# Performance work log

Hardware: AMD Instinct MI355X
Metric: run time of the kernel (lower is better)

Reference implementation:

```python
import jax, jax.numpy as jnp
import numpy as np

NG, NL, NCAM, NP, ED = 8, 4, 6, 7, 256  # groups, levels, cams, key points, embed dims
GD = ED // NG
FIX_SCALE = jnp.array([[0.0, 0.0, 0.0], [0.45, 0.0, 0.0], [-0.45, 0.0, 0.0],
                       [0.0, 0.45, 0.0], [0.0, -0.45, 0.0], [0.0, 0.0, 0.45],
                       [0.0, 0.0, -0.45]], dtype=jnp.float32)


def grid_sample_bilinear(feat, grid):
    """feat [N,C,H,W], grid [N,A,P,2] in [-1,1]; bilinear, zeros padding, align_corners=False."""
    N, C, H, W = feat.shape
    A, P = grid.shape[1], grid.shape[2]
    gx = (grid[..., 0] + 1.0) * (W * 0.5) - 0.5
    gy = (grid[..., 1] + 1.0) * (H * 0.5) - 0.5
    x0 = jnp.floor(gx)
    y0 = jnp.floor(gy)
    wx1 = gx - x0
    wy1 = gy - y0
    feat_flat = feat.reshape(N, C, H * W)

    def gather(xi, yi, w):
        valid = (xi >= 0) & (xi <= W - 1) & (yi >= 0) & (yi <= H - 1)
        xc = jnp.clip(xi, 0, W - 1).astype(jnp.int32)
        yc = jnp.clip(yi, 0, H - 1).astype(jnp.int32)
        idx = (yc * W + xc).reshape(N, 1, A * P)
        vals = jnp.take_along_axis(feat_flat, idx, axis=2)  # [N,C,A*P]
        return vals * (w * valid).reshape(N, 1, A * P)

    out = (gather(x0, y0, (1.0 - wx1) * (1.0 - wy1))
           + gather(x0 + 1.0, y0, wx1 * (1.0 - wy1))
           + gather(x0, y0 + 1.0, (1.0 - wx1) * wy1)
           + gather(x0 + 1.0, y0 + 1.0, wx1 * wy1))
    return out.reshape(N, C, A, P)


def _forward(instance_feature, anchor, anchor_embed, feat0, feat1, feat2, feat3,
             projection_mat, image_wh, w_fc, b_fc, w_out, b_out):
    B, A = anchor.shape[:2]
    # --- key point generation (box_code_size=8: size + yaw rotation + translation) ---
    size = jnp.exp(anchor[..., 3:6])[:, :, None, :]           # [B,A,1,3]
    kp = FIX_SCALE * size                                      # [B,A,7,3]
    sin, cos = anchor[..., 6], anchor[..., 7]
    z = jnp.zeros_like(cos)
    o = jnp.ones_like(cos)
    rot = jnp.stack([jnp.stack([cos, -sin, z], -1),
                     jnp.stack([sin, cos, z], -1),
                     jnp.stack([z, z, o], -1)], -2)            # [B,A,3,3]
    kp = jnp.einsum('baij,bapj->bapi', rot, kp) + anchor[..., None, 0:3]

    # --- attention weights: softmax over cams*levels*pts per group ---
    feature = instance_feature + anchor_embed
    w = feature @ w_fc.T + b_fc                                # [B,A,NG*NCAM*NL*NP]
    w = jax.nn.softmax(w.reshape(B, A, NCAM * NL * NP, NG), axis=2)
    w = w.reshape(B, A, NCAM, NL, NP, NG)

    # --- project key points to normalized image coords ---
    pts = jnp.concatenate([kp, jnp.ones_like(kp[..., :1])], -1)  # [B,A,7,4]
    p2d = jnp.einsum('bcij,bapj->bcapi', projection_mat, pts)[..., :3]
    xy = p2d[..., :2] / jnp.maximum(p2d[..., 2:3], 1e-5)
    xy = xy / jnp.maximum(image_wh[:, :, None, None], 1e-5)
    grid = (xy * 2.0 - 1.0).reshape(B * NCAM, A, NP, 2)

    # --- multilevel bilinear sampling ---
    levels = [feat0, feat1, feat2, feat3]
    sampled = jnp.stack([grid_sample_bilinear(f.reshape((B * NCAM,) + f.shape[2:]), grid)
                         for f in levels], axis=1)             # [B*Ncam,NL,C,A,P]
    feats = sampled.reshape(B, NCAM, NL, ED, A, NP).transpose(0, 4, 1, 2, 5, 3)  # [B,A,Ncam,NL,P,C]
    feats = feats.reshape(B, A, NCAM, NL, NP, NG, GD)

    # --- weighted fusion over cams, levels, then sum over key points ---
    fused = jnp.einsum('bacnpgd,bacnpg->bagd', feats, w).reshape(B, A, ED)
    return fused @ w_out.T + b_out


def setup_inputs() -> dict:
    ks = jax.random.split(jax.random.key(0), 13)
    B, A = 2, 900
    return {
        'instance_feature': jax.random.normal(ks[0], (B, A, ED), jnp.float32),
        'anchor': jax.random.normal(ks[1], (B, A, 8), jnp.float32),
        'anchor_embed': jax.random.normal(ks[2], (B, A, ED), jnp.float32),
        'feat0': jax.random.normal(ks[3], (B, NCAM, ED, 64, 176), jnp.float32),
        'feat1': jax.random.normal(ks[4], (B, NCAM, ED, 32, 88), jnp.float32),
        'feat2': jax.random.normal(ks[5], (B, NCAM, ED, 16, 44), jnp.float32),
        'feat3': jax.random.normal(ks[6], (B, NCAM, ED, 8, 22), jnp.float32),
        'projection_mat': jax.random.normal(ks[7], (B, NCAM, 4, 4), jnp.float32),
        'image_wh': jnp.ones((B, NCAM, 2), jnp.float32),
        'w_fc': jax.random.normal(ks[8], (NG * NCAM * NL * NP, ED), jnp.float32) * 0.02,
        'b_fc': jax.random.normal(ks[9], (NG * NCAM * NL * NP,), jnp.float32) * 0.02,
        'w_out': jax.random.normal(ks[10], (ED, ED), jnp.float32) * 0.02,
        'b_out': jax.random.normal(ks[11], (ED,), jnp.float32) * 0.02,
    }


def reference(instance_feature, anchor, anchor_embed, feat0, feat1, feat2, feat3,
              projection_mat, image_wh, w_fc, b_fc, w_out, b_out):
    return _forward(instance_feature, anchor, anchor_embed, feat0, feat1, feat2, feat3,
                    projection_mat, image_wh, w_fc, b_fc, w_out, b_out)
```

## Files before the change

kernel.cpp:

```cpp
#include <hip/hip_runtime.h>
#include <math.h>

constexpr int B = 2, A = 900, ED = 256, NG = 8, NCAM = 6, NL = 4, NP = 7;
constexpr int NJ = NG * NCAM * NL * NP;
constexpr int NBA = B * A;
constexpr int NE = NCAM * NL * NP;
constexpr int LDST = 260;

__constant__ float FIXS[NP][3] = {
  {0.f,0.f,0.f},{0.45f,0.f,0.f},{-0.45f,0.f,0.f},
  {0.f,0.45f,0.f},{0.f,-0.45f,0.f},{0.f,0.f,0.45f},{0.f,0.f,-0.45f}};

__constant__ int cH[NL]  = {64,32,16,8};
__constant__ int cW[NL]  = {176,88,44,22};
__constant__ int cHW[NL] = {11264,2816,704,176};
__constant__ long long cLOFF[NL] = {0LL, 0LL, 8650752LL, 10813440LL};

__global__ __launch_bounds__(256) void k_tr_cl(
    const float* __restrict__ f1, const float* __restrict__ f2,
    const float* __restrict__ f3, float* __restrict__ tfeat)
{
  __shared__ float tile[32 * LDST];
  const int bc = blockIdx.y;
  const int bx = blockIdx.x;
  int lvl, t0;
  if      (bx < 88)  { lvl = 1; t0 = 0; }
  else if (bx < 110) { lvl = 2; t0 = 88; }
  else               { lvl = 3; t0 = 110; }
  const int HW  = cHW[lvl];
  const int px0 = (bx - t0) * 32;
  const float* in = ((lvl==1)?f1:(lvl==2)?f2:f3) + (size_t)bc * ED * HW + px0;
  float* outp = tfeat + cLOFF[lvl] + ((size_t)bc * HW + px0) * ED;
  const int t = threadIdx.x;
  const int npx = min(32, HW - px0);

#pragma unroll
  for (int j = 0; j < 8; ++j) {
    const int px = 4 * j;
    if (px < npx) {
      const float4 v = *(const float4*)(in + (size_t)t * HW + px);
      tile[(px+0)*LDST + t] = v.x;
      tile[(px+1)*LDST + t] = v.y;
      tile[(px+2)*LDST + t] = v.z;
      tile[(px+3)*LDST + t] = v.w;
    }
  }
  __syncthreads();
  const int wv = t >> 6, l = t & 63;
  for (int px = wv; px < npx; px += 4) {
    const float4 v = *(const float4*)&tile[px*LDST + 4*l];
    *(float4*)(outp + (size_t)px * ED + 4*l) = v;
  }
}

__global__ __launch_bounds__(256) void k_tr(const float* __restrict__ in,
                                            float* __restrict__ out, int R, int C)
{
  __shared__ float tile[32][33];
  const int r0 = blockIdx.y * 32, c0 = blockIdx.x * 32;
  const int tx = threadIdx.x, ty = threadIdx.y;
#pragma unroll
  for (int kk = 0; kk < 4; ++kk) {
    const int r = r0 + ty + kk*8, c = c0 + tx;
    if (r < R && c < C) tile[ty + kk*8][tx] = in[(size_t)r*C + c];
  }
  __syncthreads();
#pragma unroll
  for (int kk = 0; kk < 4; ++kk) {
    const int c = c0 + ty + kk*8, r = r0 + tx;
    if (r < R && c < C) out[(size_t)c*R + r] = tile[tx][ty + kk*8];
  }
}

__global__ __launch_bounds__(192) void k_fc(const float* __restrict__ inst,
    const float* __restrict__ emb, const float* __restrict__ wt,
    const float* __restrict__ b_fc, float* __restrict__ wraw)
{
  __shared__ float fsh[8][ED];
  const int a0 = blockIdx.x * 8;
  const int j  = blockIdx.y * 192 + threadIdx.x;
  const int t  = threadIdx.x;

  for (int i = t; i < 8 * ED; i += 192) {
    const int a = i >> 8, k = i & 255;
    const size_t idx = (size_t)(a0 + a) * ED + k;
    fsh[a][k] = inst[idx] + emb[idx];
  }
  __syncthreads();

  float acc[8] = {0.f,0.f,0.f,0.f,0.f,0.f,0.f,0.f};
  for (int k = 0; k < ED; k += 4) {
    float w0 = wt[(size_t)(k+0)*NJ + j];
    float w1 = wt[(size_t)(k+1)*NJ + j];
    float w2 = wt[(size_t)(k+2)*NJ + j];
    float w3 = wt[(size_t)(k+3)*NJ + j];
#pragma unroll
    for (int a = 0; a < 8; ++a)
      acc[a] += w0*fsh[a][k] + w1*fsh[a][k+1] + w2*fsh[a][k+2] + w3*fsh[a][k+3];
  }
  const float bj = b_fc[j];
#pragma unroll
  for (int a = 0; a < 8; ++a)
    wraw[(size_t)(a0+a)*NJ + j] = acc[a] + bj;
}

template<bool CL>
__global__ __launch_bounds__(256) void k_sample_h(
    const float* __restrict__ anchor, const float* __restrict__ proj,
    const float* __restrict__ wh, const float* __restrict__ wraw,
    const float* __restrict__ tfeat,
    const float* __restrict__ f0, const float* __restrict__ f1,
    const float* __restrict__ f2, const float* __restrict__ f3,
    float* __restrict__ fused)
{
  __shared__ float wsh[NJ];
  __shared__ float gridsh[NCAM][NP][2];
  __shared__ const float* cbase[NE];
  __shared__ float4 cwt[NE];
  __shared__ int4   cmeta[NE];
  __shared__ int wcnt[4];

  const int ba = blockIdx.x;
  const int b  = ba / A;
  const int t  = threadIdx.x;

  for (int j = t; j < NJ; j += 256)
    wsh[(j & 7) * NE + (j >> 3)] = wraw[(size_t)ba*NJ + j];

  if (t < NCAM*NP) {
    const int c = t / NP, p = t % NP;
    const float* an = anchor + (size_t)ba * 8;
    const float sx = expf(an[3]), sy = expf(an[4]), sz = expf(an[5]);
    const float sn = an[6], cs = an[7];
    const float kx = FIXS[p][0]*sx, ky = FIXS[p][1]*sy, kz = FIXS[p][2]*sz;
    const float px = cs*kx - sn*ky + an[0];
    const float py = sn*kx + cs*ky + an[1];
    const float pz = kz + an[2];
    const float* P = proj + ((size_t)(b*NCAM + c))*16;
    const float X = P[0]*px + P[1]*py + P[2]*pz  + P[3];
    const float Y = P[4]*px + P[5]*py + P[6]*pz  + P[7];
    const float Z = P[8]*px + P[9]*py + P[10]*pz + P[11];
    const float zc  = fmaxf(Z, 1e-5f);
    const float whx = fmaxf(wh[(b*NCAM+c)*2+0], 1e-5f);
    const float why = fmaxf(wh[(b*NCAM+c)*2+1], 1e-5f);
    gridsh[c][p][0] = (X/zc/whx)*2.f - 1.f;
    gridsh[c][p][1] = (Y/zc/why)*2.f - 1.f;
  }
  __syncthreads();

  bool valid = false;
  int fl = 0, dx = 0, dy = 0, chstep = 0;
  float wx1 = 0.f, wy1 = 0.f;
  const float* bptr = nullptr;
  if (t < NE) {
    const int c = t / (NL*NP); const int r = t % (NL*NP);
    const int l = r / NP, p = r % NP;
    const int Wl = cW[l], Hl = cH[l], HWl = cHW[l];
    const float gx = (gridsh[c][p][0] + 1.f) * (Wl * 0.5f) - 0.5f;
    const float gy = (gridsh[c][p][1] + 1.f) * (Hl * 0.5f) - 0.5f;
    const float x0f = floorf(gx), y0f = floorf(gy);
    const bool vx0 = (x0f >=  0.f) & (x0f <= (float)(Wl-1));
    const bool vx1 = (x0f >= -1.f) & (x0f <= (float)(Wl-2));
    const bool vy0 = (y0f >=  0.f) & (y0f <= (float)(Hl-1));
    const bool vy1 = (y0f >= -1.f) & (y0f <= (float)(Hl-2));
    fl = ((vx0&&vy0)?1:0) | ((vx1&&vy0)?2:0) | ((vx0&&vy1)?4:0) | ((vx1&&vy1)?8:0);
    if (fl) {
      wx1 = gx - x0f; wy1 = gy - y0f;
      const int x0 = (int)x0f, y0 = (int)y0f;
      if (CL && l >= 1) {
        bptr = tfeat + cLOFF[l]
             + ((size_t)(b*NCAM + c) * HWl + (long long)(y0*Wl + x0)) * ED;
        chstep = 1; dx = ED; dy = Wl * ED;
      } else {
        const float* fp = (l==0)?f0:(l==1)?f1:(l==2)?f2:f3;
        bptr = fp + (size_t)(b*NCAM + c) * ED * HWl + (long long)(y0*Wl + x0);
        chstep = HWl; dx = 1; dy = Wl;
      }
      valid = true;
    }
  }

  const unsigned long long mask = __ballot(valid);
  const int lane = t & 63, wv = t >> 6;
  if (lane == 0) wcnt[wv] = __popcll(mask);
  __syncthreads();
  int off = 0, nv = 0;
#pragma unroll
  for (int i = 0; i < 4; ++i) { if (i < wv) off += wcnt[i]; nv += wcnt[i]; }
  if (valid) {
    const int pos = off + __popcll(mask & ((1ull << lane) - 1ull));
    cbase[pos] = bptr;
    cwt[pos]   = make_float4((1.f-wx1)*(1.f-wy1), wx1*(1.f-wy1),
                             (1.f-wx1)*wy1,       wx1*wy1);
    cmeta[pos] = make_int4(dx, dy, fl | (t << 8), chstep);
  }

  {
    const int g = t >> 5, ln = t & 31;
    float* wg = wsh + g * NE;
    float m = -3.4e38f;
    for (int i = ln; i < NE; i += 32) m = fmaxf(m, wg[i]);
#pragma unroll
    for (int mk = 16; mk >= 1; mk >>= 1) m = fmaxf(m, __shfl_xor(m, mk));
    float s = 0.f;
    for (int i = ln; i < NE; i += 32) {
      const float e = expf(wg[i] - m);
      wg[i] = e;
      s += e;
    }
#pragma unroll
    for (int mk = 16; mk >= 1; mk >>= 1) s += __shfl_xor(s, mk);
    const float inv = 1.f / s;
    for (int i = ln; i < NE; i += 32) wg[i] *= inv;
  }
  __syncthreads();

  float acc = 0.f;
  const int g = t >> 5;
  for (int i = 0; i < nv; ++i) {
    const int4 m = cmeta[i];
    const float* pb = cbase[i] + (size_t)t * m.w;
    const float4 w4 = cwt[i];
    const float aw = wsh[g*NE + (m.z >> 8)];
    const int f = m.z & 255;
    float sv = 0.f;
    if (f == 15) {
      sv = w4.x*pb[0] + w4.y*pb[m.x] + w4.z*pb[m.y] + w4.w*pb[m.x+m.y];
    } else {
      if (f & 1) sv += w4.x*pb[0];
      if (f & 2) sv += w4.y*pb[m.x];
      if (f & 4) sv += w4.z*pb[m.y];
      if (f & 8) sv += w4.w*pb[m.x+m.y];
    }
    acc += aw * sv;
  }
  fused[(size_t)ba*ED + t] = acc;
}

__global__ __launch_bounds__(256) void k_out(const float* __restrict__ fused,
    const float* __restrict__ w_out, const float* __restrict__ b_out,
    float* __restrict__ out)
{
  __shared__ float fsh[8][ED];
  const int a0 = blockIdx.x * 8;
  const int t = threadIdx.x;
#pragma unroll
  for (int k = 0; k < 8; ++k) fsh[k][t] = fused[(size_t)(a0+k)*ED + t];
  __syncthreads();
  float acc[8] = {0.f,0.f,0.f,0.f,0.f,0.f,0.f,0.f};
  for (int i = 0; i < ED; i += 4) {
    const float4 w4 = *(const float4*)&w_out[(size_t)t*ED + i];
#pragma unroll
    for (int k = 0; k < 8; ++k) {
      const float4 fv = *(const float4*)&fsh[k][i];
      acc[k] += w4.x*fv.x + w4.y*fv.y + w4.z*fv.z + w4.w*fv.w;
    }
  }
  const float bo = b_out[t];
#pragma unroll
  for (int k = 0; k < 8; ++k) out[(size_t)(a0+k)*ED + t] = acc[k] + bo;
}

extern "C" void kernel_launch(void* const* d_in, const int* in_sizes, int n_in,
                              void* d_out, int out_size, void* d_ws, size_t ws_size,
                              hipStream_t stream) {
  const float* inst   = (const float*)d_in[0];
  const float* anchor = (const float*)d_in[1];
  const float* emb    = (const float*)d_in[2];
  const float* f0 = (const float*)d_in[3];
  const float* f1 = (const float*)d_in[4];
  const float* f2 = (const float*)d_in[5];
  const float* f3 = (const float*)d_in[6];
  const float* proj  = (const float*)d_in[7];
  const float* wh    = (const float*)d_in[8];
  const float* w_fc  = (const float*)d_in[9];
  const float* b_fc  = (const float*)d_in[10];
  const float* w_out = (const float*)d_in[11];
  const float* b_out = (const float*)d_in[12];
  float* out = (float*)d_out;
  float* ws  = (float*)d_ws;

  const size_t TFEAT = 11354112ULL;
  const size_t WRAW  = (size_t)NBA * NJ;
  const size_t FUSED = (size_t)NBA * ED;
  const size_t WT    = (size_t)ED * NJ;
  const bool tr = ws_size >= (TFEAT + WRAW + FUSED + WT) * sizeof(float);

  float* tfeat  = ws;
  float* wraw   = tr ? (ws + TFEAT) : ws;
  float* fusedp = wraw + WRAW;
  float* wt     = fusedp + FUSED;

  k_tr<<<dim3(ED/32, NJ/32, 1), dim3(32,8), 0, stream>>>(w_fc, wt, NJ, ED);

  if (tr)
    k_tr_cl<<<dim3(116, B*NCAM), 256, 0, stream>>>(f1, f2, f3, tfeat);

  k_fc<<<dim3(NBA / 8, 7), 192, 0, stream>>>(inst, emb, wt, b_fc, wraw);

  if (tr)
    k_sample_h<true><<<NBA, 256, 0, stream>>>(anchor, proj, wh, wraw, tfeat,
                                              f0, f1, f2, f3, fusedp);
  else
    k_sample_h<false><<<NBA, 256, 0, stream>>>(anchor, proj, wh, wraw, tfeat,
                                               f0, f1, f2, f3, fusedp);

  k_out<<<NBA / 8, 256, 0, stream>>>(fusedp, w_out, b_out, out);
}
```

Measured before the change: 380.8 us.

## Split sampling kernel across two blocks per anchor and use branchless clamped corner gathers

The sampling kernel now launches two blocks per anchor, each handling half of the camera/level/point samples. Partial sums go to two separate fused buffers, which the output projection kernel adds together. The per-sample flag branches are replaced with four precomputed clamped corner pointers and zeroed weights, so the inner loop is branchless and unrolled. This gives more blocks and memory parallelism, at the cost of recomputing the softmax and grid setup in both halves, plus extra workspace and fused traffic.

```diff
diff --git a/kernel.cpp b/kernel.cpp
--- a/kernel.cpp
+++ b/kernel.cpp
@@ -6,6 +6,8 @@
 constexpr int NBA = B * A;
 constexpr int NE = NCAM * NL * NP;
 constexpr int LDST = 260;
+constexpr int SPLIT = 2;
+constexpr int EHALF = NE / SPLIT;
 
 __constant__ float FIXS[NP][3] = {
   {0.f,0.f,0.f},{0.45f,0.f,0.f},{-0.45f,0.f,0.f},
@@ -115,14 +117,15 @@
 {
   __shared__ float wsh[NJ];
   __shared__ float gridsh[NCAM][NP][2];
-  __shared__ const float* cbase[NE];
-  __shared__ float4 cwt[NE];
-  __shared__ int4   cmeta[NE];
+  __shared__ const float* cptr[EHALF][4];
+  __shared__ float4 cwt[EHALF];
+  __shared__ int2   cmeta[EHALF];
   __shared__ int wcnt[4];
 
-  const int ba = blockIdx.x;
-  const int b  = ba / A;
-  const int t  = threadIdx.x;
+  const int ba   = blockIdx.x;
+  const int half = blockIdx.y;
+  const int b    = ba / A;
+  const int t    = threadIdx.x;
 
   for (int j = t; j < NJ; j += 256)
     wsh[(j & 7) * NE + (j >> 3)] = wraw[(size_t)ba*NJ + j];
@@ -149,11 +152,12 @@
   __syncthreads();
 
   bool valid = false;
-  int fl = 0, dx = 0, dy = 0, chstep = 0;
-  float wx1 = 0.f, wy1 = 0.f;
-  const float* bptr = nullptr;
-  if (t < NE) {
-    const int c = t / (NL*NP); const int r = t % (NL*NP);
+  int chstep = 0;
+  float4 w4 = make_float4(0.f,0.f,0.f,0.f);
+  const float *p00=nullptr, *p10=nullptr, *p01=nullptr, *p11=nullptr;
+  const int e = half * EHALF + t;
+  if (t < EHALF) {
+    const int c = e / (NL*NP); const int r = e % (NL*NP);
     const int l = r / NP, p = r % NP;
     const int Wl = cW[l], Hl = cH[l], HWl = cHW[l];
     const float gx = (gridsh[c][p][0] + 1.f) * (Wl * 0.5f) - 0.5f;
@@ -163,20 +167,33 @@
     const bool vx1 = (x0f >= -1.f) & (x0f <= (float)(Wl-2));
     const bool vy0 = (y0f >=  0.f) & (y0f <= (float)(Hl-1));
     const bool vy1 = (y0f >= -1.f) & (y0f <= (float)(Hl-2));
-    fl = ((vx0&&vy0)?1:0) | ((vx1&&vy0)?2:0) | ((vx0&&vy1)?4:0) | ((vx1&&vy1)?8:0);
-    if (fl) {
-      wx1 = gx - x0f; wy1 = gy - y0f;
-      const int x0 = (int)x0f, y0 = (int)y0f;
-      if (CL && l >= 1) {
-        bptr = tfeat + cLOFF[l]
-             + ((size_t)(b*NCAM + c) * HWl + (long long)(y0*Wl + x0)) * ED;
-        chstep = 1; dx = ED; dy = Wl * ED;
-      } else {
-        const float* fp = (l==0)?f0:(l==1)?f1:(l==2)?f2:f3;
-        bptr = fp + (size_t)(b*NCAM + c) * ED * HWl + (long long)(y0*Wl + x0);
-        chstep = HWl; dx = 1; dy = Wl;
+    if (vx0|vx1|vy0|vy1) {
+      const float wx1 = gx - x0f, wy1 = gy - y0f;
+      const int x0 = (int)fmaxf(fminf(x0f,        (float)(Wl-1)), 0.f);
+      const int x1 = (int)fmaxf(fminf(x0f + 1.f,  (float)(Wl-1)), 0.f);
+      const int y0 = (int)fmaxf(fminf(y0f,        (float)(Hl-1)), 0.f);
+      const int y1 = (int)fmaxf(fminf(y0f + 1.f,  (float)(Hl-1)), 0.f);
+      w4 = make_float4((1.f-wx1)*(1.f-wy1)*(vx0&&vy0),
+                       wx1*(1.f-wy1)*(vx1&&vy0),
+                       (1.f-wx1)*wy1*(vx0&&vy1),
+                       wx1*wy1*(vx1&&vy1));
+      if (w4.x != 0.f || w4.y != 0.f || w4.z != 0.f || w4.w != 0.f) {
+        const float* base;
+        int estep;
+        if (CL && l >= 1) {
+          base = tfeat + cLOFF[l] + (size_t)(b*NCAM + c) * HWl * ED;
+          estep = ED; chstep = 1;
+        } else {
+          const float* fp = (l==0)?f0:(l==1)?f1:(l==2)?f2:f3;
+          base = fp + (size_t)(b*NCAM + c) * ED * HWl;
+          estep = 1; chstep = HWl;
+        }
+        p00 = base + (size_t)(y0*Wl + x0) * estep;
+        p10 = base + (size_t)(y0*Wl + x1) * estep;
+        p01 = base + (size_t)(y1*Wl + x0) * estep;
+        p11 = base + (size_t)(y1*Wl + x1) * estep;
+        valid = true;
       }
-      valid = true;
     }
   }
 
@@ -189,10 +206,9 @@
   for (int i = 0; i < 4; ++i) { if (i < wv) off += wcnt[i]; nv += wcnt[i]; }
   if (valid) {
     const int pos = off + __popcll(mask & ((1ull << lane) - 1ull));
-    cbase[pos] = bptr;
-    cwt[pos]   = make_float4((1.f-wx1)*(1.f-wy1), wx1*(1.f-wy1),
-                             (1.f-wx1)*wy1,       wx1*wy1);
-    cmeta[pos] = make_int4(dx, dy, fl | (t << 8), chstep);
+    cptr[pos][0] = p00; cptr[pos][1] = p10; cptr[pos][2] = p01; cptr[pos][3] = p11;
+    cwt[pos]   = w4;
+    cmeta[pos] = make_int2(chstep, e);
   }
 
   {
@@ -204,9 +220,9 @@
     for (int mk = 16; mk >= 1; mk >>= 1) m = fmaxf(m, __shfl_xor(m, mk));
     float s = 0.f;
     for (int i = ln; i < NE; i += 32) {
-      const float e = expf(wg[i] - m);
-      wg[i] = e;
-      s += e;
+      const float ev = expf(wg[i] - m);
+      wg[i] = ev;
+      s += ev;
     }
 #pragma unroll
     for (int mk = 16; mk >= 1; mk >>= 1) s += __shfl_xor(s, mk);
@@ -217,24 +233,19 @@
 
   float acc = 0.f;
   const int g = t >> 5;
+#pragma unroll 4
   for (int i = 0; i < nv; ++i) {
-    const int4 m = cmeta[i];
-    const float* pb = cbase[i] + (size_t)t * m.w;
-    const float4 w4 = cwt[i];
-    const float aw = wsh[g*NE + (m.z >> 8)];
-    const int f = m.z & 255;
-    float sv = 0.f;
-    if (f == 15) {
-      sv = w4.x*pb[0] + w4.y*pb[m.x] + w4.z*pb[m.y] + w4.w*pb[m.x+m.y];
-    } else {
-      if (f & 1) sv += w4.x*pb[0];
-      if (f & 2) sv += w4.y*pb[m.x];
-      if (f & 4) sv += w4.z*pb[m.y];
-      if (f & 8) sv += w4.w*pb[m.x+m.y];
-    }
-    acc += aw * sv;
-  }
-  fused[(size_t)ba*ED + t] = acc;
+    const int2 m = cmeta[i];
+    const size_t toff = (size_t)t * m.x;
+    const float4 w = cwt[i];
+    const float aw = wsh[g*NE + m.y];
+    const float v00 = cptr[i][0][toff];
+    const float v10 = cptr[i][1][toff];
+    const float v01 = cptr[i][2][toff];
+    const float v11 = cptr[i][3][toff];
+    acc += aw * (w.x*v00 + w.y*v10 + w.z*v01 + w.w*v11);
+  }
+  fused[((size_t)half * NBA + ba) * ED + t] = acc;
 }
 
 __global__ __launch_bounds__(256) void k_out(const float* __restrict__ fused,
@@ -245,7 +256,9 @@
   const int a0 = blockIdx.x * 8;
   const int t = threadIdx.x;
 #pragma unroll
-  for (int k = 0; k < 8; ++k) fsh[k][t] = fused[(size_t)(a0+k)*ED + t];
+  for (int k = 0; k < 8; ++k)
+    fsh[k][t] = fused[(size_t)(a0+k)*ED + t]
+              + fused[(size_t)NBA*ED + (size_t)(a0+k)*ED + t];
   __syncthreads();
   float acc[8] = {0.f,0.f,0.f,0.f,0.f,0.f,0.f,0.f};
   for (int i = 0; i < ED; i += 4) {
@@ -282,7 +295,7 @@
 
   const size_t TFEAT = 11354112ULL;
   const size_t WRAW  = (size_t)NBA * NJ;
-  const size_t FUSED = (size_t)NBA * ED;
+  const size_t FUSED = (size_t)SPLIT * NBA * ED;
   const size_t WT    = (size_t)ED * NJ;
   const bool tr = ws_size >= (TFEAT + WRAW + FUSED + WT) * sizeof(float);
 
@@ -299,11 +312,11 @@
   k_fc<<<dim3(NBA / 8, 7), 192, 0, stream>>>(inst, emb, wt, b_fc, wraw);
 
   if (tr)
-    k_sample_h<true><<<NBA, 256, 0, stream>>>(anchor, proj, wh, wraw, tfeat,
-                                              f0, f1, f2, f3, fusedp);
+    k_sample_h<true><<<dim3(NBA, SPLIT), 256, 0, stream>>>(anchor, proj, wh,
+        wraw, tfeat, f0, f1, f2, f3, fusedp);
   else
-    k_sample_h<false><<<NBA, 256, 0, stream>>>(anchor, proj, wh, wraw, tfeat,
-                                               f0, f1, f2, f3, fusedp);
+    k_sample_h<false><<<dim3(NBA, SPLIT), 256, 0, stream>>>(anchor, proj, wh,
+        wraw, tfeat, f0, f1, f2, f3, fusedp);
 
   k_out<<<NBA / 8, 256, 0, stream>>>(fusedp, w_out, b_out, out);
 }
```

After: 365.4 us. -4.0%, faster.
